# Performance work log

Measured on AMD Instinct MI355X. Metric: run time of the kernel, lower is better.

The kernel has to match this reference:

```python
import jax, jax.numpy as jnp
import numpy as np

N, F, T, H = 1024, 22, 1000, 64
EPS = 1e-5


def setup_inputs() -> dict:
    key = jax.random.key(0)
    ks = iter(jax.random.split(key, 64))
    def rn(shape, s=0.1):
        return jax.random.normal(next(ks), shape, jnp.float32) * s
    inp = {"x": rn((N, F, T), 1.0)}
    in_dims = [F, H, H]
    for l in range(3):
        inp[f"Wih{l}"] = rn((4 * H, in_dims[l]))
        inp[f"Whh{l}"] = rn((4 * H, H))
        inp[f"bih{l}"] = rn((4 * H,))
        inp[f"bhh{l}"] = rn((4 * H,))
    fc = [(64, 54), (54, 44), (44, 24), (24, 4)]
    for i, (di, do) in enumerate(fc):
        inp[f"w{i}"] = rn((do, di))
        inp[f"b{i}"] = rn((do,))
    for i, d in enumerate([54, 44, 24]):
        inp[f"g{i}"] = jnp.ones((d,), jnp.float32)
        inp[f"be{i}"] = jnp.zeros((d,), jnp.float32)
        inp[f"m{i}"] = rn((d,))
        inp[f"v{i}"] = jax.random.uniform(next(ks), (d,), jnp.float32) + 0.5
    return inp


def _lstm_layer(xs, Wih, Whh, b):
    # xs: (T, N, in) -> hs: (T, N, H)
    n = xs.shape[1]
    h0 = jnp.zeros((n, Whh.shape[1]), xs.dtype)
    def step(carry, xt):
        h, c = carry
        z = xt @ Wih.T + h @ Whh.T + b  # (N, 4H)
        i, f, g, o = jnp.split(z, 4, axis=-1)  # PyTorch gate order i,f,g,o
        c = jax.nn.sigmoid(f) * c + jax.nn.sigmoid(i) * jnp.tanh(g)
        h = jax.nn.sigmoid(o) * jnp.tanh(c)
        return (h, c), h
    (_, _), hs = jax.lax.scan(step, (h0, h0), xs)
    return hs


def _bn(x, g, be, m, v):
    return (x - m) * jax.lax.rsqrt(v + EPS) * g + be


def reference(x, Wih0, Whh0, bih0, bhh0, Wih1, Whh1, bih1, bhh1,
              Wih2, Whh2, bih2, bhh2,
              w0, b0, g0, be0, m0, v0,
              w1, b1, g1, be1, m1, v1,
              w2, b2, g2, be2, m2, v2,
              w3, b3):
    # (N, F, T) -> permute(0,2,1) -> (N, T, F); scan over time-major (T, N, F)
    xs = jnp.transpose(x, (2, 0, 1))
    xs = _lstm_layer(xs, Wih0, Whh0, bih0 + bhh0)
    xs = _lstm_layer(xs, Wih1, Whh1, bih1 + bhh1)
    xs = _lstm_layer(xs, Wih2, Whh2, bih2 + bhh2)
    h = xs[-1]  # last timestep, (N, H)
    h = jax.nn.relu(_bn(h @ w0.T + b0, g0, be0, m0, v0))
    h = jax.nn.relu(_bn(h @ w1.T + b1, g1, be1, m1, v1))
    h = jax.nn.relu(_bn(h @ w2.T + b2, g2, be2, m2, v2))
    return h @ w3.T + b3
```

## Files before the change

### kernel.cpp

```cpp
#include <hip/hip_runtime.h>
#include <hip/hip_fp16.h>

#define TT 1000
#define FF 22
#define HH 64
#define BB 4
#define NBLK 256
#define S0 112
#define S1 144
#define SL0 (4 * S0)
#define SL1 (4 * S1)

typedef _Float16 half8 __attribute__((ext_vector_type(8)));
typedef float float4v __attribute__((ext_vector_type(4)));

__device__ __forceinline__ float sel4(const float4v a, int q) {
    float lo = (q & 2) ? a[2] : a[0];
    float hi = (q & 2) ? a[3] : a[1];
    return (q & 1) ? hi : lo;
}

__device__ __forceinline__ float gate_fused(const float z[4], float& c) {
    float e0 = __expf(-z[0]);
    float e1 = __expf(-z[1]);
    float e2 = __expf(2.0f * z[2]);
    float d1 = 1.0f + e1;
    float d2 = (1.0f + e0) * (1.0f + e2);
    float r  = __builtin_amdgcn_rcpf(d1 * d2);
    float f  = d2 * r;
    float ig = (e2 - 1.0f) * (d1 * r);
    float cc = __builtin_fmaf(f, c, ig);
    c = cc;
    float e3 = __expf(-z[3]);
    float e4 = __expf(2.0f * cc);
    float r2 = __builtin_amdgcn_rcpf((1.0f + e3) * (1.0f + e4));
    return (e4 - 1.0f) * r2;
}

#define SYNC() do { asm volatile("s_waitcnt lgkmcnt(0)" ::: "memory"); \
                    __builtin_amdgcn_s_barrier(); \
                    asm volatile("" ::: "memory"); } while (0)

extern "C" __global__ void __launch_bounds__(896, 1)
lstm_fused(const float* __restrict__ x,
           const float* __restrict__ Wih0, const float* __restrict__ Whh0,
           const float* __restrict__ bih0, const float* __restrict__ bhh0,
           const float* __restrict__ Wih1, const float* __restrict__ Whh1,
           const float* __restrict__ bih1, const float* __restrict__ bhh1,
           const float* __restrict__ Wih2, const float* __restrict__ Whh2,
           const float* __restrict__ bih2, const float* __restrict__ bhh2,
           const float* __restrict__ w0, const float* __restrict__ b0,
           const float* __restrict__ w1, const float* __restrict__ b1,
           const float* __restrict__ w2, const float* __restrict__ b2,
           const float* __restrict__ w3, const float* __restrict__ b3,
           const float* __restrict__ g0, const float* __restrict__ be0,
           const float* __restrict__ m0, const float* __restrict__ v0,
           const float* __restrict__ g1, const float* __restrict__ be1,
           const float* __restrict__ m1, const float* __restrict__ v1,
           const float* __restrict__ g2, const float* __restrict__ be2,
           const float* __restrict__ m2, const float* __restrict__ v2,
           float* __restrict__ out)
{
    __shared__ __align__(16) _Float16 in0[8 * SL0];
    __shared__ __align__(16) _Float16 in1[8 * SL1];
    __shared__ __align__(16) _Float16 in2[8 * SL1];
    __shared__ float fcA[BB * 64];
    __shared__ float fcB[BB * 64];
    __shared__ float fcW[54 * 65];
    __shared__ float fcP[5 * 64];

    const int tid  = threadIdx.x;
    const int wv   = tid >> 6;
    const int role = wv >> 2;
    const int w4   = wv & 3;
    const int l    = tid & 63;
    const int q    = l >> 4;
    const int l15  = l & 15;
    const int u    = 16 * w4 + l15;
    const int b    = q;
    const int n0   = blockIdx.x * BB;

    for (int i = tid; i < 8 * SL0; i += 896) in0[i] = (_Float16)0.0f;
    for (int i = tid; i < 8 * SL1; i += 896) in1[i] = (_Float16)0.0f;
    for (int i = tid; i < 8 * SL1; i += 896) in2[i] = (_Float16)0.0f;

    half8 wf[4][4];
    float4v biasC[4];
    if (role == 2) {
#pragma unroll
        for (int g = 0; g < 4; ++g) {
            const int row = 64 * g + u;
#pragma unroll
            for (int kt = 0; kt < 3; ++kt) {
                half8 h{};
#pragma unroll
                for (int j = 0; j < 8; ++j) {
                    const int k = 32 * kt + 8 * q + j;
                    float val = 0.0f;
                    if (k < 32) { if (k < FF) val = Wih0[row * FF + k]; }
                    else        { val = Whh0[row * HH + (k - 32)]; }
                    h[j] = (_Float16)val;
                }
                wf[g][kt] = h;
            }
            float bv = bih0[row] + bhh0[row];
            biasC[g] = float4v{bv, bv, bv, bv};
        }
    } else if (role < 2) {
        const float* Wih = role ? Wih1 : Wih2;
        const float* Whh = role ? Whh1 : Whh2;
        const float* bih = role ? bih1 : bih2;
        const float* bhh = role ? bhh1 : bhh2;
#pragma unroll
        for (int g = 0; g < 4; ++g) {
            const int row = 64 * g + u;
#pragma unroll
            for (int kt = 0; kt < 4; ++kt) {
                half8 h{};
#pragma unroll
                for (int j = 0; j < 8; ++j) {
                    const int k = 32 * kt + 8 * q + j;
                    h[j] = (_Float16)((k < 64) ? Wih[row * HH + k] : Whh[row * HH + (k - 64)]);
                }
                wf[g][kt] = h;
            }
            float bv = bih[row] + bhh[row];
            biasC[g] = float4v{bv, bv, bv, bv};
        }
    }

    const int  st  = tid - 768;
    const bool xok = (role == 3) && (st >= 0) && (st < BB * FF);
    const int  xb  = xok ? (st / FF) : 0;
    const int  xf  = xok ? (st - xb * FF) : 0;
    const float* xp = x + ((size_t)(n0 + xb) * FF + xf) * TT;

    __syncthreads();

    float xA = xok ? xp[0] : 0.f;
    float xB = xok ? xp[1] : 0.f;

    const int arow = (role == 2) ? ((l15 & 3) * S0 + q * 8) : ((l15 & 3) * S1 + q * 8);
    float c = 0.f;
    float4v acc[4] = {};

    for (int k = 0; k < 126; ++k) {
#pragma unroll
        for (int s = 0; s < 8; ++s) {
            const int n = 8 * k + s;

            SYNC();
            if (role == 3) {
                if (n <= TT - 1) {
                    if (xok) in0[s * SL0 + xb * S0 + xf] = (_Float16)xA;
                    xA = xB;
                    if (xok) {
                        int tn = n + 2; if (tn > TT - 1) tn = TT - 1;
                        xB = xp[tn];
                    }
                }
            } else if (role == 2) {
                if (n >= 1 && n <= TT) {
                    float z[4];
#pragma unroll
                    for (int g = 0; g < 4; ++g) z[g] = sel4(acc[g], q);
                    float h = gate_fused(z, c);
                    _Float16 hf = (_Float16)h;
                    in0[s * SL0 + b * S0 + 32 + u]          = hf;
                    in1[((s + 7) & 7) * SL1 + b * S1 + u]   = hf;
                }
            } else if (role == 1) {
                if (n >= 2 && n <= TT + 1) {
                    float z[4];
#pragma unroll
                    for (int g = 0; g < 4; ++g) z[g] = sel4(acc[g], q);
                    float h = gate_fused(z, c);
                    _Float16 hf = (_Float16)h;
                    in1[((s + 7) & 7) * SL1 + b * S1 + 64 + u] = hf;
                    in2[((s + 6) & 7) * SL1 + b * S1 + u]      = hf;
                }
            } else {
                if (n >= 3 && n <= TT + 2) {
                    const _Float16* rd = in2 + ((s + 5) & 7) * SL1;
                    half8 a0 = *(const half8*)(rd + arow);
                    half8 a1 = *(const half8*)(rd + arow + 32);
                    half8 a2 = *(const half8*)(rd + arow + 64);
                    half8 a3 = *(const half8*)(rd + arow + 96);
#pragma unroll
                    for (int g = 0; g < 4; ++g)
                        acc[g] = __builtin_amdgcn_mfma_f32_16x16x32_f16(a0, wf[g][0], biasC[g], 0, 0, 0);
#pragma unroll
                    for (int g = 0; g < 4; ++g)
                        acc[g] = __builtin_amdgcn_mfma_f32_16x16x32_f16(a1, wf[g][1], acc[g], 0, 0, 0);
#pragma unroll
                    for (int g = 0; g < 4; ++g)
                        acc[g] = __builtin_amdgcn_mfma_f32_16x16x32_f16(a2, wf[g][2], acc[g], 0, 0, 0);
#pragma unroll
                    for (int g = 0; g < 4; ++g)
                        acc[g] = __builtin_amdgcn_mfma_f32_16x16x32_f16(a3, wf[g][3], acc[g], 0, 0, 0);
                }
            }

            SYNC();
            if (role == 2) {
                if (n <= TT - 1) {
                    const _Float16* rd = in0 + s * SL0;
                    half8 a0 = *(const half8*)(rd + arow);
                    half8 a1 = *(const half8*)(rd + arow + 32);
                    half8 a2 = *(const half8*)(rd + arow + 64);
#pragma unroll
                    for (int g = 0; g < 4; ++g)
                        acc[g] = __builtin_amdgcn_mfma_f32_16x16x32_f16(a0, wf[g][0], biasC[g], 0, 0, 0);
#pragma unroll
                    for (int g = 0; g < 4; ++g)
                        acc[g] = __builtin_amdgcn_mfma_f32_16x16x32_f16(a1, wf[g][1], acc[g], 0, 0, 0);
#pragma unroll
                    for (int g = 0; g < 4; ++g)
                        acc[g] = __builtin_amdgcn_mfma_f32_16x16x32_f16(a2, wf[g][2], acc[g], 0, 0, 0);
                }
            } else if (role == 1) {
                if (n >= 1 && n <= TT) {
                    const _Float16* rd = in1 + ((s + 7) & 7) * SL1;
                    half8 a0 = *(const half8*)(rd + arow);
                    half8 a1 = *(const half8*)(rd + arow + 32);
                    half8 a2 = *(const half8*)(rd + arow + 64);
                    half8 a3 = *(const half8*)(rd + arow + 96);
#pragma unroll
                    for (int g = 0; g < 4; ++g)
                        acc[g] = __builtin_amdgcn_mfma_f32_16x16x32_f16(a0, wf[g][0], biasC[g], 0, 0, 0);
#pragma unroll
                    for (int g = 0; g < 4; ++g)
                        acc[g] = __builtin_amdgcn_mfma_f32_16x16x32_f16(a1, wf[g][1], acc[g], 0, 0, 0);
#pragma unroll
                    for (int g = 0; g < 4; ++g)
                        acc[g] = __builtin_amdgcn_mfma_f32_16x16x32_f16(a2, wf[g][2], acc[g], 0, 0, 0);
#pragma unroll
                    for (int g = 0; g < 4; ++g)
                        acc[g] = __builtin_amdgcn_mfma_f32_16x16x32_f16(a3, wf[g][3], acc[g], 0, 0, 0);
                }
            } else if (role == 0) {
                if (n >= 3 && n <= TT + 2) {
                    float z[4];
#pragma unroll
                    for (int g = 0; g < 4; ++g) z[g] = sel4(acc[g], q);
                    float h = gate_fused(z, c);
                    if (n != TT + 2) {
                        in2[((s + 6) & 7) * SL1 + b * S1 + 64 + u] = (_Float16)h;
                    } else {
                        fcA[b * 64 + u] = h;
                    }
                }
            }
        }
    }

    __syncthreads();

    for (int i = tid; i < 54 * 64; i += 896) fcW[(i >> 6) * 65 + (i & 63)] = w0[i];
    for (int i = tid; i < 54; i += 896) {
        fcP[i] = b0[i]; fcP[64 + i] = g0[i]; fcP[128 + i] = be0[i];
        fcP[192 + i] = m0[i]; fcP[256 + i] = v0[i];
    }
    __syncthreads();
    for (int idx = tid; idx < BB * 54; idx += 896) {
        const int bb = idx / 54, j = idx - bb * 54;
        float s = fcP[j];
        for (int k = 0; k < 64; ++k) s += fcW[j * 65 + k] * fcA[bb * 64 + k];
        s = (s - fcP[192 + j]) * rsqrtf(fcP[256 + j] + 1e-5f) * fcP[64 + j] + fcP[128 + j];
        fcB[bb * 64 + j] = fmaxf(s, 0.0f);
    }
    __syncthreads();

    for (int i = tid; i < 44 * 54; i += 896) fcW[(i / 54) * 55 + (i % 54)] = w1[i];
    for (int i = tid; i < 44; i += 896) {
        fcP[i] = b1[i]; fcP[64 + i] = g1[i]; fcP[128 + i] = be1[i];
        fcP[192 + i] = m1[i]; fcP[256 + i] = v1[i];
    }
    __syncthreads();
    for (int idx = tid; idx < BB * 44; idx += 896) {
        const int bb = idx / 44, j = idx - bb * 44;
        float s = fcP[j];
        for (int k = 0; k < 54; ++k) s += fcW[j * 55 + k] * fcB[bb * 64 + k];
        s = (s - fcP[192 + j]) * rsqrtf(fcP[256 + j] + 1e-5f) * fcP[64 + j] + fcP[128 + j];
        fcA[bb * 64 + j] = fmaxf(s, 0.0f);
    }
    __syncthreads();

    for (int i = tid; i < 24 * 44; i += 896) fcW[(i / 44) * 45 + (i % 44)] = w2[i];
    for (int i = tid; i < 24; i += 896) {
        fcP[i] = b2[i]; fcP[64 + i] = g2[i]; fcP[128 + i] = be2[i];
        fcP[192 + i] = m2[i]; fcP[256 + i] = v2[i];
    }
    __syncthreads();
    for (int idx = tid; idx < BB * 24; idx += 896) {
        const int bb = idx / 24, j = idx - bb * 24;
        float s = fcP[j];
        for (int k = 0; k < 44; ++k) s += fcW[j * 45 + k] * fcA[bb * 64 + k];
        s = (s - fcP[192 + j]) * rsqrtf(fcP[256 + j] + 1e-5f) * fcP[64 + j] + fcP[128 + j];
        fcB[bb * 64 + j] = fmaxf(s, 0.0f);
    }
    __syncthreads();

    for (int i = tid; i < 4 * 24; i += 896) fcW[(i / 24) * 25 + (i % 24)] = w3[i];
    for (int i = tid; i < 4; i += 896) fcP[i] = b3[i];
    __syncthreads();
    for (int idx = tid; idx < BB * 4; idx += 896) {
        const int bb = idx / 4, j = idx - bb * 4;
        float s = fcP[j];
        for (int k = 0; k < 24; ++k) s += fcW[j * 25 + k] * fcB[bb * 64 + k];
        out[(size_t)(n0 + bb) * 4 + j] = s;
    }
}

extern "C" void kernel_launch(void* const* d_in, const int* in_sizes, int n_in,
                              void* d_out, int out_size, void* d_ws, size_t ws_size,
                              hipStream_t stream) {
    const float* p[33];
    for (int i = 0; i < 33; ++i) p[i] = (const float*)d_in[i];
    lstm_fused<<<NBLK, 896, 0, stream>>>(
        p[0],
        p[1], p[2], p[3], p[4],
        p[5], p[6], p[7], p[8],
        p[9], p[10], p[11], p[12],
        p[13], p[14], p[15], p[16], p[17], p[18], p[19], p[20],
        p[21], p[22], p[23], p[24],
        p[25], p[26], p[27], p[28],
        p[29], p[30], p[31], p[32],
        (float*)d_out);
}
```

Baseline: 946.2 us.

## Merge MFMA and gate phases into one barrier per step, drop loader wave

Restructures the wavefront-pipelined three-layer LSTM so that each time step uses a single barrier instead of two. Each role now computes its MFMAs and gate nonlinearity in the same phase, and prefetches the next step's recurrent operand right after the barrier. The dedicated x-loading warp group is removed; layer-0 waves stream x themselves, and the block shrinks from 896 to 768 threads. The bias moves from the MFMA accumulator init to a scalar add after the reduction. In exchange, pipeline skew and buffer indexing change, which risks subtle off-by-one errors, and the longer per-step critical path inside each phase may offset the saved barrier.

After: 877.5 us. 7.3% less time.

```diff
diff --git a/kernel.cpp b/kernel.cpp
--- a/kernel.cpp
+++ b/kernel.cpp
@@ -41,7 +41,7 @@
                     __builtin_amdgcn_s_barrier(); \
                     asm volatile("" ::: "memory"); } while (0)
 
-extern "C" __global__ void __launch_bounds__(896, 1)
+extern "C" __global__ void __launch_bounds__(768, 1)
 lstm_fused(const float* __restrict__ x,
            const float* __restrict__ Wih0, const float* __restrict__ Whh0,
            const float* __restrict__ bih0, const float* __restrict__ bhh0,
@@ -80,12 +80,12 @@
     const int b    = q;
     const int n0   = blockIdx.x * BB;
 
-    for (int i = tid; i < 8 * SL0; i += 896) in0[i] = (_Float16)0.0f;
-    for (int i = tid; i < 8 * SL1; i += 896) in1[i] = (_Float16)0.0f;
-    for (int i = tid; i < 8 * SL1; i += 896) in2[i] = (_Float16)0.0f;
+    for (int i = tid; i < 8 * SL0; i += 768) in0[i] = (_Float16)0.0f;
+    for (int i = tid; i < 8 * SL1; i += 768) in1[i] = (_Float16)0.0f;
+    for (int i = tid; i < 8 * SL1; i += 768) in2[i] = (_Float16)0.0f;
 
     half8 wf[4][4];
-    float4v biasC[4];
+    float bv[4];
     if (role == 2) {
 #pragma unroll
         for (int g = 0; g < 4; ++g) {
@@ -103,10 +103,10 @@
                 }
                 wf[g][kt] = h;
             }
-            float bv = bih0[row] + bhh0[row];
-            biasC[g] = float4v{bv, bv, bv, bv};
+            wf[g][3] = half8{};
+            bv[g] = bih0[row] + bhh0[row];
         }
-    } else if (role < 2) {
+    } else {
         const float* Wih = role ? Wih1 : Wih2;
         const float* Whh = role ? Whh1 : Whh2;
         const float* bih = role ? bih1 : bih2;
@@ -124,128 +124,139 @@
                 }
                 wf[g][kt] = h;
             }
-            float bv = bih[row] + bhh[row];
-            biasC[g] = float4v{bv, bv, bv, bv};
+            bv[g] = bih[row] + bhh[row];
         }
     }
 
-    const int  st  = tid - 768;
-    const bool xok = (role == 3) && (st >= 0) && (st < BB * FF);
-    const int  xb  = xok ? (st / FF) : 0;
-    const int  xf  = xok ? (st - xb * FF) : 0;
-    const float* xp = x + ((size_t)(n0 + xb) * FF + xf) * TT;
-
-    __syncthreads();
-
-    float xA = xok ? xp[0] : 0.f;
-    float xB = xok ? xp[1] : 0.f;
+    const bool xok = (role == 2) && (l < FF);
+    const int  xb  = w4;
+    const float* xp = x + ((size_t)(n0 + xb) * FF + l) * TT;
+
+    __syncthreads();
+
+    if (xok) {
+        in0[0 * SL0 + xb * S0 + l] = (_Float16)xp[0];
+        in0[1 * SL0 + xb * S0 + l] = (_Float16)xp[1];
+    }
+    float xA = xok ? xp[2] : 0.f;
+    float xB = xok ? xp[3] : 0.f;
+
+    __syncthreads();
 
     const int arow = (role == 2) ? ((l15 & 3) * S0 + q * 8) : ((l15 & 3) * S1 + q * 8);
     float c = 0.f;
-    float4v acc[4] = {};
+    const float4v zz = {0.f, 0.f, 0.f, 0.f};
+
+    half8 pre0{}, pre1{};
+    if (role == 2) pre0 = *(const half8*)(in0 + arow);
 
     for (int k = 0; k < 126; ++k) {
 #pragma unroll
         for (int s = 0; s < 8; ++s) {
-            const int n = 8 * k + s;
-
+            const int tau = 8 * k + s;
             SYNC();
-            if (role == 3) {
-                if (n <= TT - 1) {
-                    if (xok) in0[s * SL0 + xb * S0 + xf] = (_Float16)xA;
-                    xA = xB;
-                    if (xok) {
-                        int tn = n + 2; if (tn > TT - 1) tn = TT - 1;
-                        xB = xp[tn];
-                    }
-                }
-            } else if (role == 2) {
-                if (n >= 1 && n <= TT) {
+
+            if (role == 2) {
+                const bool act = (tau <= TT - 1);
+                float4v A[4];
+                if (act) {
+                    const _Float16* rd = in0 + s * SL0;
+                    half8 a1 = *(const half8*)(rd + arow + 32);
+                    half8 a2 = *(const half8*)(rd + arow + 64);
+#pragma unroll
+                    for (int g = 0; g < 4; ++g)
+                        A[g] = __builtin_amdgcn_mfma_f32_16x16x32_f16(pre0, wf[g][0], zz, 0, 0, 0);
+#pragma unroll
+                    for (int g = 0; g < 4; ++g)
+                        A[g] = __builtin_amdgcn_mfma_f32_16x16x32_f16(a1, wf[g][1], A[g], 0, 0, 0);
+#pragma unroll
+                    for (int g = 0; g < 4; ++g)
+                        A[g] = __builtin_amdgcn_mfma_f32_16x16x32_f16(a2, wf[g][2], A[g], 0, 0, 0);
+                }
+                pre0 = *(const half8*)(in0 + ((s + 1) & 7) * SL0 + arow);
+                if (act) {
                     float z[4];
 #pragma unroll
-                    for (int g = 0; g < 4; ++g) z[g] = sel4(acc[g], q);
+                    for (int g = 0; g < 4; ++g) z[g] = sel4(A[g], q) + bv[g];
                     float h = gate_fused(z, c);
                     _Float16 hf = (_Float16)h;
-                    in0[s * SL0 + b * S0 + 32 + u]          = hf;
-                    in1[((s + 7) & 7) * SL1 + b * S1 + u]   = hf;
+                    in0[((s + 1) & 7) * SL0 + b * S0 + 32 + u] = hf;
+                    in1[s * SL1 + b * S1 + u]                  = hf;
+                }
+                if (xok && tau <= TT - 3)
+                    in0[((s + 2) & 7) * SL0 + xb * S0 + l] = (_Float16)xA;
+                xA = xB;
+                if (xok) {
+                    int tn = tau + 4; if (tn > TT - 1) tn = TT - 1;
+                    xB = xp[tn];
                 }
             } else if (role == 1) {
-                if (n >= 2 && n <= TT + 1) {
+                const bool act = (tau >= 2) && (tau <= TT + 1);
+                float4v A[4];
+                if (act) {
+                    const _Float16* rd = in2  , *rr = in1 + ((s + 6) & 7) * SL1;
+                    (void)rd;
+                    half8 a2 = *(const half8*)(rr + arow + 64);
+                    half8 a3 = *(const half8*)(rr + arow + 96);
+#pragma unroll
+                    for (int g = 0; g < 4; ++g)
+                        A[g] = __builtin_amdgcn_mfma_f32_16x16x32_f16(pre0, wf[g][0], zz, 0, 0, 0);
+#pragma unroll
+                    for (int g = 0; g < 4; ++g)
+                        A[g] = __builtin_amdgcn_mfma_f32_16x16x32_f16(pre1, wf[g][1], A[g], 0, 0, 0);
+#pragma unroll
+                    for (int g = 0; g < 4; ++g)
+                        A[g] = __builtin_amdgcn_mfma_f32_16x16x32_f16(a2, wf[g][2], A[g], 0, 0, 0);
+#pragma unroll
+                    for (int g = 0; g < 4; ++g)
+                        A[g] = __builtin_amdgcn_mfma_f32_16x16x32_f16(a3, wf[g][3], A[g], 0, 0, 0);
+                }
+                {
+                    const _Float16* rn = in1 + ((s + 7) & 7) * SL1;
+                    pre0 = *(const half8*)(rn + arow);
+                    pre1 = *(const half8*)(rn + arow + 32);
+                }
+                if (act) {
                     float z[4];
 #pragma unroll
-                    for (int g = 0; g < 4; ++g) z[g] = sel4(acc[g], q);
+                    for (int g = 0; g < 4; ++g) z[g] = sel4(A[g], q) + bv[g];
                     float h = gate_fused(z, c);
                     _Float16 hf = (_Float16)h;
                     in1[((s + 7) & 7) * SL1 + b * S1 + 64 + u] = hf;
                     in2[((s + 6) & 7) * SL1 + b * S1 + u]      = hf;
                 }
             } else {
-                if (n >= 3 && n <= TT + 2) {
-                    const _Float16* rd = in2 + ((s + 5) & 7) * SL1;
-                    half8 a0 = *(const half8*)(rd + arow);
-                    half8 a1 = *(const half8*)(rd + arow + 32);
-                    half8 a2 = *(const half8*)(rd + arow + 64);
-                    half8 a3 = *(const half8*)(rd + arow + 96);
-#pragma unroll
-                    for (int g = 0; g < 4; ++g)
-                        acc[g] = __builtin_amdgcn_mfma_f32_16x16x32_f16(a0, wf[g][0], biasC[g], 0, 0, 0);
-#pragma unroll
-                    for (int g = 0; g < 4; ++g)
-                        acc[g] = __builtin_amdgcn_mfma_f32_16x16x32_f16(a1, wf[g][1], acc[g], 0, 0, 0);
-#pragma unroll
-                    for (int g = 0; g < 4; ++g)
-                        acc[g] = __builtin_amdgcn_mfma_f32_16x16x32_f16(a2, wf[g][2], acc[g], 0, 0, 0);
-#pragma unroll
-                    for (int g = 0; g < 4; ++g)
-                        acc[g] = __builtin_amdgcn_mfma_f32_16x16x32_f16(a3, wf[g][3], acc[g], 0, 0, 0);
-                }
-            }
-
-            SYNC();
-            if (role == 2) {
-                if (n <= TT - 1) {
-                    const _Float16* rd = in0 + s * SL0;
-                    half8 a0 = *(const half8*)(rd + arow);
-                    half8 a1 = *(const half8*)(rd + arow + 32);
-                    half8 a2 = *(const half8*)(rd + arow + 64);
-#pragma unroll
-                    for (int g = 0; g < 4; ++g)
-                        acc[g] = __builtin_amdgcn_mfma_f32_16x16x32_f16(a0, wf[g][0], biasC[g], 0, 0, 0);
-#pragma unroll
-                    for (int g = 0; g < 4; ++g)
-                        acc[g] = __builtin_amdgcn_mfma_f32_16x16x32_f16(a1, wf[g][1], acc[g], 0, 0, 0);
-#pragma unroll
-                    for (int g = 0; g < 4; ++g)
-                        acc[g] = __builtin_amdgcn_mfma_f32_16x16x32_f16(a2, wf[g][2], acc[g], 0, 0, 0);
-                }
-            } else if (role == 1) {
-                if (n >= 1 && n <= TT) {
-                    const _Float16* rd = in1 + ((s + 7) & 7) * SL1;
-                    half8 a0 = *(const half8*)(rd + arow);
-                    half8 a1 = *(const half8*)(rd + arow + 32);
-                    half8 a2 = *(const half8*)(rd + arow + 64);
-                    half8 a3 = *(const half8*)(rd + arow + 96);
-#pragma unroll
-                    for (int g = 0; g < 4; ++g)
-                        acc[g] = __builtin_amdgcn_mfma_f32_16x16x32_f16(a0, wf[g][0], biasC[g], 0, 0, 0);
-#pragma unroll
-                    for (int g = 0; g < 4; ++g)
-                        acc[g] = __builtin_amdgcn_mfma_f32_16x16x32_f16(a1, wf[g][1], acc[g], 0, 0, 0);
-#pragma unroll
-                    for (int g = 0; g < 4; ++g)
-                        acc[g] = __builtin_amdgcn_mfma_f32_16x16x32_f16(a2, wf[g][2], acc[g], 0, 0, 0);
-#pragma unroll
-                    for (int g = 0; g < 4; ++g)
-                        acc[g] = __builtin_amdgcn_mfma_f32_16x16x32_f16(a3, wf[g][3], acc[g], 0, 0, 0);
-                }
-            } else if (role == 0) {
-                if (n >= 3 && n <= TT + 2) {
+                const bool act = (tau >= 4) && (tau <= TT + 3);
+                float4v A[4];
+                if (act) {
+                    const _Float16* rr = in2 + ((s + 4) & 7) * SL1;
+                    half8 a2 = *(const half8*)(rr + arow + 64);
+                    half8 a3 = *(const half8*)(rr + arow + 96);
+#pragma unroll
+                    for (int g = 0; g < 4; ++g)
+                        A[g] = __builtin_amdgcn_mfma_f32_16x16x32_f16(pre0, wf[g][0], zz, 0, 0, 0);
+#pragma unroll
+                    for (int g = 0; g < 4; ++g)
+                        A[g] = __builtin_amdgcn_mfma_f32_16x16x32_f16(pre1, wf[g][1], A[g], 0, 0, 0);
+#pragma unroll
+                    for (int g = 0; g < 4; ++g)
+                        A[g] = __builtin_amdgcn_mfma_f32_16x16x32_f16(a2, wf[g][2], A[g], 0, 0, 0);
+#pragma unroll
+                    for (int g = 0; g < 4; ++g)
+                        A[g] = __builtin_amdgcn_mfma_f32_16x16x32_f16(a3, wf[g][3], A[g], 0, 0, 0);
+                }
+                {
+                    const _Float16* rn = in2 + ((s + 5) & 7) * SL1;
+                    pre0 = *(const half8*)(rn + arow);
+                    pre1 = *(const half8*)(rn + arow + 32);
+                }
+                if (act) {
                     float z[4];
 #pragma unroll
-                    for (int g = 0; g < 4; ++g) z[g] = sel4(acc[g], q);
+                    for (int g = 0; g < 4; ++g) z[g] = sel4(A[g], q) + bv[g];
                     float h = gate_fused(z, c);
-                    if (n != TT + 2) {
-                        in2[((s + 6) & 7) * SL1 + b * S1 + 64 + u] = (_Float16)h;
+                    if (tau != TT + 3) {
+                        in2[((s + 5) & 7) * SL1 + b * S1 + 64 + u] = (_Float16)h;
                     } else {
                         fcA[b * 64 + u] = h;
                     }
@@ -256,13 +267,13 @@
 
     __syncthreads();
 
-    for (int i = tid; i < 54 * 64; i += 896) fcW[(i >> 6) * 65 + (i & 63)] = w0[i];
-    for (int i = tid; i < 54; i += 896) {
+    for (int i = tid; i < 54 * 64; i += 768) fcW[(i >> 6) * 65 + (i & 63)] = w0[i];
+    for (int i = tid; i < 54; i += 768) {
         fcP[i] = b0[i]; fcP[64 + i] = g0[i]; fcP[128 + i] = be0[i];
         fcP[192 + i] = m0[i]; fcP[256 + i] = v0[i];
     }
     __syncthreads();
-    for (int idx = tid; idx < BB * 54; idx += 896) {
+    for (int idx = tid; idx < BB * 54; idx += 768) {
         const int bb = idx / 54, j = idx - bb * 54;
         float s = fcP[j];
         for (int k = 0; k < 64; ++k) s += fcW[j * 65 + k] * fcA[bb * 64 + k];
@@ -271,13 +282,13 @@
     }
     __syncthreads();
 
-    for (int i = tid; i < 44 * 54; i += 896) fcW[(i / 54) * 55 + (i % 54)] = w1[i];
-    for (int i = tid; i < 44; i += 896) {
+    for (int i = tid; i < 44 * 54; i += 768) fcW[(i / 54) * 55 + (i % 54)] = w1[i];
+    for (int i = tid; i < 44; i += 768) {
         fcP[i] = b1[i]; fcP[64 + i] = g1[i]; fcP[128 + i] = be1[i];
         fcP[192 + i] = m1[i]; fcP[256 + i] = v1[i];
     }
     __syncthreads();
-    for (int idx = tid; idx < BB * 44; idx += 896) {
+    for (int idx = tid; idx < BB * 44; idx += 768) {
         const int bb = idx / 44, j = idx - bb * 44;
         float s = fcP[j];
         for (int k = 0; k < 54; ++k) s += fcW[j * 55 + k] * fcB[bb * 64 + k];
@@ -286,13 +297,13 @@
     }
     __syncthreads();
 
-    for (int i = tid; i < 24 * 44; i += 896) fcW[(i / 44) * 45 + (i % 44)] = w2[i];
-    for (int i = tid; i < 24; i += 896) {
+    for (int i = tid; i < 24 * 44; i += 768) fcW[(i / 44) * 45 + (i % 44)] = w2[i];
+    for (int i = tid; i < 24; i += 768) {
         fcP[i] = b2[i]; fcP[64 + i] = g2[i]; fcP[128 + i] = be2[i];
         fcP[192 + i] = m2[i]; fcP[256 + i] = v2[i];
     }
     __syncthreads();
-    for (int idx = tid; idx < BB * 24; idx += 896) {
+    for (int idx = tid; idx < BB * 24; idx += 768) {
         const int bb = idx / 24, j = idx - bb * 24;
         float s = fcP[j];
         for (int k = 0; k < 44; ++k) s += fcW[j * 45 + k] * fcA[bb * 64 + k];
@@ -301,10 +312,10 @@
     }
     __syncthreads();
 
-    for (int i = tid; i < 4 * 24; i += 896) fcW[(i / 24) * 25 + (i % 24)] = w3[i];
-    for (int i = tid; i < 4; i += 896) fcP[i] = b3[i];
-    __syncthreads();
-    for (int idx = tid; idx < BB * 4; idx += 896) {
+    for (int i = tid; i < 4 * 24; i += 768) fcW[(i / 24) * 25 + (i % 24)] = w3[i];
+    for (int i = tid; i < 4; i += 768) fcP[i] = b3[i];
+    __syncthreads();
+    for (int idx = tid; idx < BB * 4; idx += 768) {
         const int bb = idx / 4, j = idx - bb * 4;
         float s = fcP[j];
         for (int k = 0; k < 24; ++k) s += fcW[j * 25 + k] * fcB[bb * 64 + k];
@@ -317,7 +328,7 @@
                               hipStream_t stream) {
     const float* p[33];
     for (int i = 0; i < 33; ++i) p[i] = (const float*)d_in[i];
-    lstm_fused<<<NBLK, 896, 0, stream>>>(
+    lstm_fused<<<NBLK, 768, 0, stream>>>(
         p[0],
         p[1], p[2], p[3], p[4],
         p[5], p[6], p[7], p[8],
```

## Collapse two barriers per step into one with software-pipelined input MFMAs

Applied to the files above, without the earlier changes.

Restructures the wavefront-specialized LSTM pipeline so each timestep uses a single barrier instead of two. The input-projection MFMAs for the next step are issued right after the gate computation, since they do not depend on the recurrent state. After the barrier, only the recurrent-part MFMAs and the gates remain on the critical path. Bias is now added after the MFMAs rather than used as the accumulator seed, and x is prefetched two steps further ahead. This changes buffer index offsets and layer lags, which adds risk of off-by-one errors in the ring-buffer slots.

New measurement: 780.9 us. -17.5%, faster.

```diff
diff --git a/kernel.cpp b/kernel.cpp
--- a/kernel.cpp
+++ b/kernel.cpp
@@ -40,6 +40,7 @@
 #define SYNC() do { asm volatile("s_waitcnt lgkmcnt(0)" ::: "memory"); \
                     __builtin_amdgcn_s_barrier(); \
                     asm volatile("" ::: "memory"); } while (0)
+#define SB()   __builtin_amdgcn_sched_barrier(0)
 
 extern "C" __global__ void __launch_bounds__(896, 1)
 lstm_fused(const float* __restrict__ x,
@@ -85,7 +86,7 @@
     for (int i = tid; i < 8 * SL1; i += 896) in2[i] = (_Float16)0.0f;
 
     half8 wf[4][4];
-    float4v biasC[4];
+    float bv[4];
     if (role == 2) {
 #pragma unroll
         for (int g = 0; g < 4; ++g) {
@@ -103,8 +104,8 @@
                 }
                 wf[g][kt] = h;
             }
-            float bv = bih0[row] + bhh0[row];
-            biasC[g] = float4v{bv, bv, bv, bv};
+            wf[g][3] = half8{};
+            bv[g] = bih0[row] + bhh0[row];
         }
     } else if (role < 2) {
         const float* Wih = role ? Wih1 : Wih2;
@@ -124,8 +125,7 @@
                 }
                 wf[g][kt] = h;
             }
-            float bv = bih[row] + bhh[row];
-            biasC[g] = float4v{bv, bv, bv, bv};
+            bv[g] = bih[row] + bhh[row];
         }
     }
 
@@ -137,120 +137,151 @@
 
     __syncthreads();
 
-    float xA = xok ? xp[0] : 0.f;
-    float xB = xok ? xp[1] : 0.f;
+    if (xok) {
+        in0[0 * SL0 + xb * S0 + xf] = (_Float16)xp[0];
+        in0[1 * SL0 + xb * S0 + xf] = (_Float16)xp[1];
+    }
+    float xA = xok ? xp[2] : 0.f;
+    float xB = xok ? xp[3] : 0.f;
+
+    __syncthreads();
 
     const int arow = (role == 2) ? ((l15 & 3) * S0 + q * 8) : ((l15 & 3) * S1 + q * 8);
     float c = 0.f;
-    float4v acc[4] = {};
+    const float4v zz = {0.f, 0.f, 0.f, 0.f};
+    float4v acc[4] = {zz, zz, zz, zz};
+
+    if (role == 2) {
+        half8 f0 = *(const half8*)(in0 + 0 * SL0 + arow);
+#pragma unroll
+        for (int g = 0; g < 4; ++g)
+            acc[g] = __builtin_amdgcn_mfma_f32_16x16x32_f16(f0, wf[g][0], zz, 0, 0, 0);
+    }
 
     for (int k = 0; k < 126; ++k) {
 #pragma unroll
         for (int s = 0; s < 8; ++s) {
-            const int n = 8 * k + s;
-
+            const int tau = 8 * k + s;
             SYNC();
+
             if (role == 3) {
-                if (n <= TT - 1) {
-                    if (xok) in0[s * SL0 + xb * S0 + xf] = (_Float16)xA;
+                if (tau <= TT - 3) {
+                    if (xok) in0[((s + 2) & 7) * SL0 + xb * S0 + xf] = (_Float16)xA;
                     xA = xB;
                     if (xok) {
-                        int tn = n + 2; if (tn > TT - 1) tn = TT - 1;
+                        int tn = tau + 4; if (tn > TT - 1) tn = TT - 1;
                         xB = xp[tn];
                     }
                 }
             } else if (role == 2) {
-                if (n >= 1 && n <= TT) {
+                const bool act  = (tau <= TT - 1);
+                const bool actn = (tau <= TT - 2);
+                half8 f0{};
+                if (act) {
+                    const _Float16* rd = in0 + s * SL0;
+                    half8 r1 = *(const half8*)(rd + arow + 32);
+                    half8 r2 = *(const half8*)(rd + arow + 64);
+#pragma unroll
+                    for (int g = 0; g < 4; ++g)
+                        acc[g] = __builtin_amdgcn_mfma_f32_16x16x32_f16(r1, wf[g][1], acc[g], 0, 0, 0);
+#pragma unroll
+                    for (int g = 0; g < 4; ++g)
+                        acc[g] = __builtin_amdgcn_mfma_f32_16x16x32_f16(r2, wf[g][2], acc[g], 0, 0, 0);
+                }
+                if (actn)
+                    f0 = *(const half8*)(in0 + ((s + 1) & 7) * SL0 + arow);
+                if (act) {
                     float z[4];
 #pragma unroll
-                    for (int g = 0; g < 4; ++g) z[g] = sel4(acc[g], q);
+                    for (int g = 0; g < 4; ++g) z[g] = sel4(acc[g], q) + bv[g];
                     float h = gate_fused(z, c);
                     _Float16 hf = (_Float16)h;
-                    in0[s * SL0 + b * S0 + 32 + u]          = hf;
-                    in1[((s + 7) & 7) * SL1 + b * S1 + u]   = hf;
+                    in0[((s + 1) & 7) * SL0 + b * S0 + 32 + u] = hf;
+                    in1[s * SL1 + b * S1 + u]                  = hf;
+                }
+                if (actn) {
+#pragma unroll
+                    for (int g = 0; g < 4; ++g)
+                        acc[g] = __builtin_amdgcn_mfma_f32_16x16x32_f16(f0, wf[g][0], zz, 0, 0, 0);
                 }
             } else if (role == 1) {
-                if (n >= 2 && n <= TT + 1) {
+                const bool act  = (tau >= 2) && (tau <= TT + 1);
+                const bool actn = (tau >= 1) && (tau <= TT);
+                half8 f0{}, f1{};
+                if (act) {
+                    const _Float16* rr = in1 + ((s + 6) & 7) * SL1;
+                    half8 r2 = *(const half8*)(rr + arow + 64);
+                    half8 r3 = *(const half8*)(rr + arow + 96);
+#pragma unroll
+                    for (int g = 0; g < 4; ++g)
+                        acc[g] = __builtin_amdgcn_mfma_f32_16x16x32_f16(r2, wf[g][2], acc[g], 0, 0, 0);
+#pragma unroll
+                    for (int g = 0; g < 4; ++g)
+                        acc[g] = __builtin_amdgcn_mfma_f32_16x16x32_f16(r3, wf[g][3], acc[g], 0, 0, 0);
+                }
+                if (actn) {
+                    const _Float16* rn = in1 + ((s + 7) & 7) * SL1;
+                    f0 = *(const half8*)(rn + arow);
+                    f1 = *(const half8*)(rn + arow + 32);
+                }
+                if (act) {
                     float z[4];
 #pragma unroll
-                    for (int g = 0; g < 4; ++g) z[g] = sel4(acc[g], q);
+                    for (int g = 0; g < 4; ++g) z[g] = sel4(acc[g], q) + bv[g];
                     float h = gate_fused(z, c);
                     _Float16 hf = (_Float16)h;
                     in1[((s + 7) & 7) * SL1 + b * S1 + 64 + u] = hf;
                     in2[((s + 6) & 7) * SL1 + b * S1 + u]      = hf;
                 }
+                if (actn) {
+#pragma unroll
+                    for (int g = 0; g < 4; ++g)
+                        acc[g] = __builtin_amdgcn_mfma_f32_16x16x32_f16(f0, wf[g][0], zz, 0, 0, 0);
+#pragma unroll
+                    for (int g = 0; g < 4; ++g)
+                        acc[g] = __builtin_amdgcn_mfma_f32_16x16x32_f16(f1, wf[g][1], acc[g], 0, 0, 0);
+                }
             } else {
-                if (n >= 3 && n <= TT + 2) {
-                    const _Float16* rd = in2 + ((s + 5) & 7) * SL1;
-                    half8 a0 = *(const half8*)(rd + arow);
-                    half8 a1 = *(const half8*)(rd + arow + 32);
-                    half8 a2 = *(const half8*)(rd + arow + 64);
-                    half8 a3 = *(const half8*)(rd + arow + 96);
-#pragma unroll
-                    for (int g = 0; g < 4; ++g)
-                        acc[g] = __builtin_amdgcn_mfma_f32_16x16x32_f16(a0, wf[g][0], biasC[g], 0, 0, 0);
-#pragma unroll
-                    for (int g = 0; g < 4; ++g)
-                        acc[g] = __builtin_amdgcn_mfma_f32_16x16x32_f16(a1, wf[g][1], acc[g], 0, 0, 0);
-#pragma unroll
-                    for (int g = 0; g < 4; ++g)
-                        acc[g] = __builtin_amdgcn_mfma_f32_16x16x32_f16(a2, wf[g][2], acc[g], 0, 0, 0);
-#pragma unroll
-                    for (int g = 0; g < 4; ++g)
-                        acc[g] = __builtin_amdgcn_mfma_f32_16x16x32_f16(a3, wf[g][3], acc[g], 0, 0, 0);
-                }
-            }
-
-            SYNC();
-            if (role == 2) {
-                if (n <= TT - 1) {
-                    const _Float16* rd = in0 + s * SL0;
-                    half8 a0 = *(const half8*)(rd + arow);
-                    half8 a1 = *(const half8*)(rd + arow + 32);
-                    half8 a2 = *(const half8*)(rd + arow + 64);
-#pragma unroll
-                    for (int g = 0; g < 4; ++g)
-                        acc[g] = __builtin_amdgcn_mfma_f32_16x16x32_f16(a0, wf[g][0], biasC[g], 0, 0, 0);
-#pragma unroll
-                    for (int g = 0; g < 4; ++g)
-                        acc[g] = __builtin_amdgcn_mfma_f32_16x16x32_f16(a1, wf[g][1], acc[g], 0, 0, 0);
-#pragma unroll
-                    for (int g = 0; g < 4; ++g)
-                        acc[g] = __builtin_amdgcn_mfma_f32_16x16x32_f16(a2, wf[g][2], acc[g], 0, 0, 0);
-                }
-            } else if (role == 1) {
-                if (n >= 1 && n <= TT) {
-                    const _Float16* rd = in1 + ((s + 7) & 7) * SL1;
-                    half8 a0 = *(const half8*)(rd + arow);
-                    half8 a1 = *(const half8*)(rd + arow + 32);
-                    half8 a2 = *(const half8*)(rd + arow + 64);
-                    half8 a3 = *(const half8*)(rd + arow + 96);
-#pragma unroll
-                    for (int g = 0; g < 4; ++g)
-                        acc[g] = __builtin_amdgcn_mfma_f32_16x16x32_f16(a0, wf[g][0], biasC[g], 0, 0, 0);
-#pragma unroll
-                    for (int g = 0; g < 4; ++g)
-                        acc[g] = __builtin_amdgcn_mfma_f32_16x16x32_f16(a1, wf[g][1], acc[g], 0, 0, 0);
-#pragma unroll
-                    for (int g = 0; g < 4; ++g)
-                        acc[g] = __builtin_amdgcn_mfma_f32_16x16x32_f16(a2, wf[g][2], acc[g], 0, 0, 0);
-#pragma unroll
-                    for (int g = 0; g < 4; ++g)
-                        acc[g] = __builtin_amdgcn_mfma_f32_16x16x32_f16(a3, wf[g][3], acc[g], 0, 0, 0);
-                }
-            } else if (role == 0) {
-                if (n >= 3 && n <= TT + 2) {
+                const bool act  = (tau >= 4) && (tau <= TT + 3);
+                const bool actn = (tau >= 3) && (tau <= TT + 2);
+                half8 f0{}, f1{};
+                if (act) {
+                    const _Float16* rr = in2 + ((s + 4) & 7) * SL1;
+                    half8 r2 = *(const half8*)(rr + arow + 64);
+                    half8 r3 = *(const half8*)(rr + arow + 96);
+#pragma unroll
+                    for (int g = 0; g < 4; ++g)
+                        acc[g] = __builtin_amdgcn_mfma_f32_16x16x32_f16(r2, wf[g][2], acc[g], 0, 0, 0);
+#pragma unroll
+                    for (int g = 0; g < 4; ++g)
+                        acc[g] = __builtin_amdgcn_mfma_f32_16x16x32_f16(r3, wf[g][3], acc[g], 0, 0, 0);
+                }
+                if (actn) {
+                    const _Float16* rn = in2 + ((s + 5) & 7) * SL1;
+                    f0 = *(const half8*)(rn + arow);
+                    f1 = *(const half8*)(rn + arow + 32);
+                }
+                if (act) {
                     float z[4];
 #pragma unroll
-                    for (int g = 0; g < 4; ++g) z[g] = sel4(acc[g], q);
+                    for (int g = 0; g < 4; ++g) z[g] = sel4(acc[g], q) + bv[g];
                     float h = gate_fused(z, c);
-                    if (n != TT + 2) {
-                        in2[((s + 6) & 7) * SL1 + b * S1 + 64 + u] = (_Float16)h;
+                    if (tau != TT + 3) {
+                        in2[((s + 5) & 7) * SL1 + b * S1 + 64 + u] = (_Float16)h;
                     } else {
                         fcA[b * 64 + u] = h;
                     }
                 }
+                if (actn) {
+#pragma unroll
+                    for (int g = 0; g < 4; ++g)
+                        acc[g] = __builtin_amdgcn_mfma_f32_16x16x32_f16(f0, wf[g][0], zz, 0, 0, 0);
+#pragma unroll
+                    for (int g = 0; g < 4; ++g)
+                        acc[g] = __builtin_amdgcn_mfma_f32_16x16x32_f16(f1, wf[g][1], acc[g], 0, 0, 0);
+                }
             }
+            SB();
         }
     }
 
```
